# Kernel optimization log

Measured on AMD Instinct MI355X. Metric: run time of the kernel, lower is better.

## Reference

```python
import jax, jax.numpy as jnp
import numpy as np

B = 16384

def _linear_params(key, out_dim, in_dim):
    k1, k2 = jax.random.split(key)
    s = 1.0 / np.sqrt(in_dim)
    W = jax.random.uniform(k1, (out_dim, in_dim), jnp.float32, -s, s)
    b = jax.random.uniform(k2, (out_dim,), jnp.float32, -s, s)
    return W, b

def setup_inputs() -> dict:
    key = jax.random.key(0)
    ks = jax.random.split(key, 6)
    x = jax.random.normal(ks[0], (B, 784), jnp.float32)
    conv_w = jax.random.normal(ks[1], (3, 3), jnp.float32)
    W1, b1 = _linear_params(ks[2], 1024, 26 * 26)
    W2, b2 = _linear_params(ks[3], 512, 1024)
    W3, b3 = _linear_params(ks[4], 256, 512)
    W4, b4 = _linear_params(ks[5], 10, 256)
    return {"x": x, "conv_w": conv_w, "W1": W1, "b1": b1, "W2": W2, "b2": b2,
            "W3": W3, "b3": b3, "W4": W4, "b4": b4}

def reference(x, conv_w, W1, b1, W2, b2, W3, b3, W4, b4):
    b = x.shape[0]
    img = x.reshape(b, 1, 28, 28)                       # NCHW
    kern = conv_w.reshape(1, 1, 3, 3)                   # OIHW; cross-correlation
    y = jax.lax.conv_general_dilated(img, kern, (1, 1), 'VALID')  # [B,1,26,26]
    h = y.reshape(b, 26 * 26)
    h = jax.nn.relu(h @ W1.T + b1)
    h = jax.nn.relu(h @ W2.T + b2)
    h = jax.nn.relu(h @ W3.T + b3)
    return h @ W4.T + b4                                # [B,10] logits
```

## Files before the change

### kernel.cpp

```cpp
#include <hip/hip_runtime.h>
#include <hip/hip_bf16.h>
#include <stdint.h>

#define BDIM 256

typedef __attribute__((ext_vector_type(8))) short short8;
typedef __attribute__((ext_vector_type(4))) float f32x4;

#define AS1 __attribute__((address_space(1)))
#define AS3 __attribute__((address_space(3)))
#define GLL16(g, s) __builtin_amdgcn_global_load_lds((AS1 const void*)(g), (AS3 void*)(s), 16, 0, 0)

__device__ __forceinline__ unsigned short f2bf(float f) {
  union { float f; unsigned u; } v; v.f = f;
  unsigned r = v.u + 0x7fffu + ((v.u >> 16) & 1u);
  return (unsigned short)(r >> 16);
}
__device__ __forceinline__ float bf2f(unsigned short u) {
  union { unsigned u; float f; } v; v.u = ((unsigned)u) << 16;
  return v.f;
}

template <int N> __device__ __forceinline__ void vmwait() {
  static_assert(N == 0 || N == 4 || N == 6 || N == 8, "unsupported vmcnt");
  if constexpr (N == 8)      asm volatile("s_waitcnt vmcnt(8)" ::: "memory");
  else if constexpr (N == 6) asm volatile("s_waitcnt vmcnt(6)" ::: "memory");
  else if constexpr (N == 4) asm volatile("s_waitcnt vmcnt(4)" ::: "memory");
  else                       asm volatile("s_waitcnt vmcnt(0)" ::: "memory");
  __builtin_amdgcn_sched_barrier(0);
}

__global__ __launch_bounds__(BDIM) void cast_pad_w1(const float* __restrict__ w,
                                                    unsigned short* __restrict__ o) {
  int idx = blockIdx.x * BDIM + threadIdx.x;
  if (idx >= 1024 * 704) return;
  int n = idx / 704, k = idx - n * 704;
  float v = (k < 676) ? w[n * 676 + k] : 0.f;
  o[idx] = f2bf(v);
}

__global__ __launch_bounds__(BDIM) void cast_plain(const float* __restrict__ w,
                                                   unsigned short* __restrict__ o, int count) {
  int idx = blockIdx.x * BDIM + threadIdx.x;
  if (idx < count) o[idx] = f2bf(w[idx]);
}

__global__ __launch_bounds__(BDIM) void conv3x3(const float* __restrict__ x,
                                                const float* __restrict__ cw,
                                                unsigned short* __restrict__ h0) {
  __shared__ float xs[784];
  __shared__ float w[9];
  int m = blockIdx.x;
  const float* xr = x + (size_t)m * 784;
  if (threadIdx.x < 9) w[threadIdx.x] = cw[threadIdx.x];
  for (int i = threadIdx.x; i < 784; i += BDIM) xs[i] = xr[i];
  __syncthreads();
  unsigned short* hr = h0 + (size_t)m * 704;
  for (int p = threadIdx.x; p < 704; p += BDIM) {
    float v = 0.f;
    if (p < 676) {
      int r = p / 26, c = p - r * 26;
      const float* xp = &xs[r * 28 + c];
      v = xp[0]  * w[0] + xp[1]  * w[1] + xp[2]  * w[2]
        + xp[28] * w[3] + xp[29] * w[4] + xp[30] * w[5]
        + xp[56] * w[6] + xp[57] * w[7] + xp[58] * w[8];
    }
    hr[p] = f2bf(v);
  }
}

template <int BM, int BN, int WGM, bool RELU>
__global__ __launch_bounds__(512, 2) void gemm_bt2(const unsigned short* __restrict__ A,
                                                   const unsigned short* __restrict__ Wt,
                                                   const float* __restrict__ bias,
                                                   unsigned short* __restrict__ Cb,
                                                   int M, int N, int K) {
  constexpr int WGN = 8 / WGM;
  constexpr int FM = BM / WGM / 16;
  constexpr int FN = BN / WGN / 16;
  constexpr int RA = BM / 64;
  constexpr int RB = BN / 64;
  constexpr int LPT = RA + RB;
  __shared__ unsigned short lds[(size_t)(BM + BN) * 128];
  unsigned short* const Asb = lds;
  unsigned short* const Bsb = lds + 2 * BM * 64;

  const int tid = threadIdx.x;
  const int lane = tid & 63;
  const int wid = tid >> 6;
  const int nbm = M / BM;
  const int brow = (blockIdx.x % nbm) * BM;
  const int bcol = (blockIdx.x / nbm) * BN;

  const int srow = tid >> 3;
  const int sslot = (tid & 7) ^ (srow & 7);
  const unsigned short* gA = A + (size_t)(brow + srow) * K + sslot * 8;
  const unsigned short* gB = Wt + (size_t)(bcol + srow) * K + sslot * 8;
  const int sdst = tid * 8;

#define STAGE(buf, kt)                                                            \
  do {                                                                            \
    _Pragma("unroll")                                                             \
    for (int r = 0; r < RA; ++r)                                                  \
      GLL16(gA + (size_t)r * 64 * K + (size_t)(kt) * 64,                          \
            Asb + (buf) * BM * 64 + r * 4096 + sdst);                             \
    _Pragma("unroll")                                                             \
    for (int r = 0; r < RB; ++r)                                                  \
      GLL16(gB + (size_t)r * 64 * K + (size_t)(kt) * 64,                          \
            Bsb + (buf) * BN * 64 + r * 4096 + sdst);                             \
  } while (0)

  f32x4 acc[FM][FN] = {};

  const int fr = lane & 15;
  const int h = lane >> 4;
  const int fx = fr & 7;
  const int abase = (wid / WGN) * (FM * 16);
  const int bbase = (wid % WGN) * (FN * 16);

  const int nk = K >> 6;
  STAGE(0, 0);
  STAGE(1, 1);
  int cur = 0;
  for (int kt = 0; kt < nk; ++kt) {
    if (kt + 1 < nk) vmwait<LPT>();
    else             vmwait<0>();
    __builtin_amdgcn_s_barrier();
    __builtin_amdgcn_sched_barrier(0);
    __builtin_amdgcn_s_setprio(1);
#pragma unroll
    for (int s = 0; s < 2; ++s) {
      const int slot = (((s << 2) + h) ^ fx) << 3;
      short8 af[FM], bf[FN];
#pragma unroll
      for (int m = 0; m < FM; ++m)
        af[m] = *(const short8*)&Asb[cur * BM * 64 + (abase + m * 16 + fr) * 64 + slot];
#pragma unroll
      for (int n = 0; n < FN; ++n)
        bf[n] = *(const short8*)&Bsb[cur * BN * 64 + (bbase + n * 16 + fr) * 64 + slot];
#pragma unroll
      for (int m = 0; m < FM; ++m)
#pragma unroll
        for (int n = 0; n < FN; ++n)
          acc[m][n] = __builtin_amdgcn_mfma_f32_16x16x32_bf16(af[m], bf[n], acc[m][n], 0, 0, 0);
    }
    __builtin_amdgcn_s_setprio(0);
    __builtin_amdgcn_sched_barrier(0);
    __builtin_amdgcn_s_barrier();
    __builtin_amdgcn_sched_barrier(0);
    if (kt + 2 < nk) STAGE(cur, kt + 2);
    cur ^= 1;
  }
#undef STAGE

  unsigned short* const scr = lds;
  const int lrow0 = abase + (h << 2);
  const int lcol0 = bbase + fr;
#pragma unroll
  for (int n = 0; n < FN; ++n) {
    const int col = lcol0 + n * 16;
    const float bv = bias[bcol + col];
#pragma unroll
    for (int m = 0; m < FM; ++m) {
#pragma unroll
      for (int j = 0; j < 4; ++j) {
        const int row = lrow0 + m * 16 + j;
        float v = acc[m][n][j] + bv;
        if (RELU) v = v > 0.f ? v : 0.f;
        scr[(row * BN + col) ^ ((row & 12) << 2)] = f2bf(v);
      }
    }
  }
  __syncthreads();
  constexpr int CPR = BN / 8;
  constexpr int TOT = BM * CPR;
#pragma unroll 2
  for (int i = tid; i < TOT; i += 512) {
    const int row = i / CPR, c = i % CPR;
    const int cs = c ^ ((row & 12) >> 1);
    short8 vv = *(const short8*)&scr[row * BN + cs * 8];
    *(short8*)(Cb + (size_t)(brow + row) * N + bcol + c * 8) = vv;
  }
}

__global__ __launch_bounds__(BDIM) void fc10(const unsigned short* __restrict__ h3,
                                             const float* __restrict__ W4,
                                             const float* __restrict__ b4,
                                             float* __restrict__ out) {
  int lane = threadIdx.x & 63;
  int wid = threadIdx.x >> 6;
  int m = blockIdx.x * 4 + wid;
  const unsigned short* hr = h3 + (size_t)m * 256 + lane * 4;
  uint64_t hv = *(const uint64_t*)hr;
  float e0 = bf2f((unsigned short)hv), e1 = bf2f((unsigned short)(hv >> 16));
  float e2 = bf2f((unsigned short)(hv >> 32)), e3 = bf2f((unsigned short)(hv >> 48));
#pragma unroll
  for (int n = 0; n < 10; ++n) {
    const float4 wv = *(const float4*)(W4 + n * 256 + lane * 4);
    float s = e0 * wv.x + e1 * wv.y + e2 * wv.z + e3 * wv.w;
#pragma unroll
    for (int off = 32; off > 0; off >>= 1) s += __shfl_xor(s, off);
    if (lane == n) out[(size_t)m * 10 + n] = s + b4[n];
  }
}

extern "C" void kernel_launch(void* const* d_in, const int* in_sizes, int n_in,
                              void* d_out, int out_size, void* d_ws, size_t ws_size,
                              hipStream_t stream) {
  const float* x  = (const float*)d_in[0];
  const float* cw = (const float*)d_in[1];
  const float* W1 = (const float*)d_in[2];
  const float* b1 = (const float*)d_in[3];
  const float* W2 = (const float*)d_in[4];
  const float* b2 = (const float*)d_in[5];
  const float* W3 = (const float*)d_in[6];
  const float* b3 = (const float*)d_in[7];
  const float* W4 = (const float*)d_in[8];
  const float* b4 = (const float*)d_in[9];
  float* out = (float*)d_out;

  char* ws = (char*)d_ws;
  unsigned short* h0  = (unsigned short*)(ws);
  unsigned short* h1  = (unsigned short*)(ws + 23068672);
  unsigned short* W1b = (unsigned short*)(ws + 23068672 + 33554432);
  unsigned short* W2b = W1b + 1024 * 704;
  unsigned short* W3b = W2b + 512 * 1024;
  unsigned short* h2  = h0;
  unsigned short* h3  = h1;

  cast_pad_w1<<<2816, BDIM, 0, stream>>>(W1, W1b);
  cast_plain<<<2048, BDIM, 0, stream>>>(W2, W2b, 512 * 1024);
  cast_plain<<<512, BDIM, 0, stream>>>(W3, W3b, 256 * 512);
  conv3x3<<<16384, BDIM, 0, stream>>>(x, cw, h0);

  gemm_bt2<256, 256, 2, true><<<(16384 / 256) * (1024 / 256), 512, 0, stream>>>(
      h0, W1b, b1, h1, 16384, 1024, 704);
  gemm_bt2<256, 128, 4, true><<<(16384 / 256) * (512 / 128), 512, 0, stream>>>(
      h1, W2b, b2, h2, 16384, 512, 1024);
  gemm_bt2<128, 128, 4, true><<<(16384 / 128) * (256 / 128), 512, 0, stream>>>(
      h2, W3b, b3, h3, 16384, 256, 512);
  fc10<<<16384 / 4, BDIM, 0, stream>>>(h3, W4, b4, out);
}
```

Before: 112.8 us.

## Split GEMM k-step into phases interleaving staged loads with MFMA groups

Restructures the GEMM main loop into 2 or 4 phases per k-tile. The A tile for the next step is issued early, and the B tile halves for step k+2 are spread across phases, with a barrier pair per phase. The aim is to overlap global-to-LDS transfers with MFMA work and to cut the single long wait and barrier stall per iteration. In exchange it adds more barriers per k-step and makes the vmcnt accounting more delicate.

Result: no change. 111.7 us (-1.0%).

```diff
diff --git a/kernel.cpp b/kernel.cpp
--- a/kernel.cpp
+++ b/kernel.cpp
@@ -22,10 +22,11 @@
 }
 
 template <int N> __device__ __forceinline__ void vmwait() {
-  static_assert(N == 0 || N == 4 || N == 6 || N == 8, "unsupported vmcnt");
+  static_assert(N == 0 || N == 2 || N == 4 || N == 6 || N == 8, "unsupported vmcnt");
   if constexpr (N == 8)      asm volatile("s_waitcnt vmcnt(8)" ::: "memory");
   else if constexpr (N == 6) asm volatile("s_waitcnt vmcnt(6)" ::: "memory");
   else if constexpr (N == 4) asm volatile("s_waitcnt vmcnt(4)" ::: "memory");
+  else if constexpr (N == 2) asm volatile("s_waitcnt vmcnt(2)" ::: "memory");
   else                       asm volatile("s_waitcnt vmcnt(0)" ::: "memory");
   __builtin_amdgcn_sched_barrier(0);
 }
@@ -70,7 +71,7 @@
 }
 
 template <int BM, int BN, int WGM, bool RELU>
-__global__ __launch_bounds__(512, 2) void gemm_bt2(const unsigned short* __restrict__ A,
+__global__ __launch_bounds__(512, 2) void gemm_bt3(const unsigned short* __restrict__ A,
                                                    const unsigned short* __restrict__ Wt,
                                                    const float* __restrict__ bias,
                                                    unsigned short* __restrict__ Cb,
@@ -80,7 +81,8 @@
   constexpr int FN = BN / WGN / 16;
   constexpr int RA = BM / 64;
   constexpr int RB = BN / 64;
-  constexpr int LPT = RA + RB;
+  constexpr int NPH = (FM == 8) ? 4 : 2;
+  constexpr int MPG = FM / NPH;
   __shared__ unsigned short lds[(size_t)(BM + BN) * 128];
   unsigned short* const Asb = lds;
   unsigned short* const Bsb = lds + 2 * BM * 64;
@@ -98,20 +100,20 @@
   const unsigned short* gB = Wt + (size_t)(bcol + srow) * K + sslot * 8;
   const int sdst = tid * 8;
 
-#define STAGE(buf, kt)                                                            \
-  do {                                                                            \
-    _Pragma("unroll")                                                             \
-    for (int r = 0; r < RA; ++r)                                                  \
-      GLL16(gA + (size_t)r * 64 * K + (size_t)(kt) * 64,                          \
-            Asb + (buf) * BM * 64 + r * 4096 + sdst);                             \
-    _Pragma("unroll")                                                             \
-    for (int r = 0; r < RB; ++r)                                                  \
-      GLL16(gB + (size_t)r * 64 * K + (size_t)(kt) * 64,                          \
-            Bsb + (buf) * BN * 64 + r * 4096 + sdst);                             \
+#define STAGE_A(buf, kt)                                                      \
+  do { _Pragma("unroll")                                                      \
+    for (int r = 0; r < RA; ++r)                                              \
+      GLL16(gA + (size_t)r * 64 * K + (size_t)(kt) * 64,                      \
+            Asb + (buf) * BM * 64 + r * 4096 + sdst);                         \
   } while (0)
+#define STAGE_BH(buf, kt, hh)                                                 \
+  do { _Pragma("unroll")                                                      \
+    for (int r = (hh) * (RB / 2); r < ((hh) + 1) * (RB / 2); ++r)             \
+      GLL16(gB + (size_t)r * 64 * K + (size_t)(kt) * 64,                      \
+            Bsb + (buf) * BN * 64 + r * 4096 + sdst);                         \
+  } while (0)
 
   f32x4 acc[FM][FN] = {};
-
   const int fr = lane & 15;
   const int h = lane >> 4;
   const int fx = fr & 7;
@@ -119,39 +121,64 @@
   const int bbase = (wid % WGN) * (FN * 16);
 
   const int nk = K >> 6;
-  STAGE(0, 0);
-  STAGE(1, 1);
-  int cur = 0;
+  STAGE_A(0, 0);
+  STAGE_BH(0, 0, 0); STAGE_BH(0, 0, 1);
+  STAGE_BH(1, 1, 0); STAGE_BH(1, 1, 1);
+  vmwait<RB>();
+  __builtin_amdgcn_s_barrier();
+  __builtin_amdgcn_sched_barrier(0);
+
   for (int kt = 0; kt < nk; ++kt) {
-    if (kt + 1 < nk) vmwait<LPT>();
-    else             vmwait<0>();
-    __builtin_amdgcn_s_barrier();
-    __builtin_amdgcn_sched_barrier(0);
-    __builtin_amdgcn_s_setprio(1);
-#pragma unroll
-    for (int s = 0; s < 2; ++s) {
-      const int slot = (((s << 2) + h) ^ fx) << 3;
-      short8 af[FM], bf[FN];
-#pragma unroll
-      for (int m = 0; m < FM; ++m)
-        af[m] = *(const short8*)&Asb[cur * BM * 64 + (abase + m * 16 + fr) * 64 + slot];
-#pragma unroll
-      for (int n = 0; n < FN; ++n)
-        bf[n] = *(const short8*)&Bsb[cur * BN * 64 + (bbase + n * 16 + fr) * 64 + slot];
-#pragma unroll
-      for (int m = 0; m < FM; ++m)
+    const int cur = kt & 1;
+    const unsigned short* As0 = Asb + cur * BM * 64;
+    const unsigned short* Bs0 = Bsb + cur * BN * 64;
+    short8 bf[FN][2];
+#pragma unroll
+    for (int ph = 0; ph < NPH; ++ph) {
+      if (ph == 0) {
 #pragma unroll
         for (int n = 0; n < FN; ++n)
-          acc[m][n] = __builtin_amdgcn_mfma_f32_16x16x32_bf16(af[m], bf[n], acc[m][n], 0, 0, 0);
+#pragma unroll
+          for (int s = 0; s < 2; ++s)
+            bf[n][s] = *(const short8*)&Bs0[(bbase + n * 16 + fr) * 64 + ((((s << 2) + h) ^ fx) << 3)];
+      }
+      short8 af[MPG][2];
+#pragma unroll
+      for (int mm = 0; mm < MPG; ++mm)
+#pragma unroll
+        for (int s = 0; s < 2; ++s)
+          af[mm][s] = *(const short8*)&As0[(abase + (ph * MPG + mm) * 16 + fr) * 64 + ((((s << 2) + h) ^ fx) << 3)];
+      if (ph == 0) { if (kt + 1 < nk) STAGE_A(cur ^ 1, kt + 1); }
+      if (NPH == 4) {
+        if (ph == 1 && kt + 2 < nk) STAGE_BH(cur, kt + 2, 0);
+        if (ph == 2 && kt + 2 < nk) STAGE_BH(cur, kt + 2, 1);
+      } else {
+        if (ph == 1 && kt + 2 < nk) { STAGE_BH(cur, kt + 2, 0); STAGE_BH(cur, kt + 2, 1); }
+      }
+      __builtin_amdgcn_sched_barrier(0);
+      __builtin_amdgcn_s_barrier();
+      __builtin_amdgcn_sched_barrier(0);
+      __builtin_amdgcn_s_setprio(1);
+#pragma unroll
+      for (int s = 0; s < 2; ++s)
+#pragma unroll
+        for (int mm = 0; mm < MPG; ++mm)
+#pragma unroll
+          for (int n = 0; n < FN; ++n)
+            acc[ph * MPG + mm][n] =
+                __builtin_amdgcn_mfma_f32_16x16x32_bf16(af[mm][s], bf[n][s], acc[ph * MPG + mm][n], 0, 0, 0);
+      __builtin_amdgcn_s_setprio(0);
+      __builtin_amdgcn_sched_barrier(0);
+      if (ph == NPH - 1) {
+        if (kt + 2 < nk) vmwait<RB>();
+        else             vmwait<0>();
+      }
+      __builtin_amdgcn_s_barrier();
+      __builtin_amdgcn_sched_barrier(0);
     }
-    __builtin_amdgcn_s_setprio(0);
-    __builtin_amdgcn_sched_barrier(0);
-    __builtin_amdgcn_s_barrier();
-    __builtin_amdgcn_sched_barrier(0);
-    if (kt + 2 < nk) STAGE(cur, kt + 2);
-    cur ^= 1;
-  }
-#undef STAGE
+  }
+#undef STAGE_A
+#undef STAGE_BH
 
   unsigned short* const scr = lds;
   const int lrow0 = abase + (h << 2);
@@ -233,11 +260,11 @@
   cast_plain<<<512, BDIM, 0, stream>>>(W3, W3b, 256 * 512);
   conv3x3<<<16384, BDIM, 0, stream>>>(x, cw, h0);
 
-  gemm_bt2<256, 256, 2, true><<<(16384 / 256) * (1024 / 256), 512, 0, stream>>>(
+  gemm_bt3<256, 256, 2, true><<<(16384 / 256) * (1024 / 256), 512, 0, stream>>>(
       h0, W1b, b1, h1, 16384, 1024, 704);
-  gemm_bt2<256, 128, 4, true><<<(16384 / 256) * (512 / 128), 512, 0, stream>>>(
+  gemm_bt3<256, 128, 4, true><<<(16384 / 256) * (512 / 128), 512, 0, stream>>>(
       h1, W2b, b2, h2, 16384, 512, 1024);
-  gemm_bt2<128, 128, 4, true><<<(16384 / 128) * (256 / 128), 512, 0, stream>>>(
+  gemm_bt3<128, 128, 4, true><<<(16384 / 128) * (256 / 128), 512, 0, stream>>>(
       h2, W3b, b3, h3, 16384, 256, 512);
   fc10<<<16384 / 4, BDIM, 0, stream>>>(h3, W4, b4, out);
 }
```
